# Performance work log

Measured on AMD Instinct MI355X. Metric: run time of the kernel, lower is better.

## Reference

```python
import jax, jax.numpy as jnp
import numpy as np
import math

B = 512
EMB = 512
CLASSNUM = 70722
M = 0.4
H = 0.333
S = 64.0
EPS = 1e-3


def setup_inputs() -> dict:
    key = jax.random.key(0)
    k1, k2, k3, k4, k5 = jax.random.split(key, 5)
    embbedings = jax.random.normal(k1, (B, EMB), dtype=jnp.float32)
    # feature norms: positive, realistic range ~[1, 30)
    norms = jax.random.uniform(k2, (B, 1), dtype=jnp.float32) * 29.0 + 1.0
    label = jax.random.randint(k3, (B,), 0, CLASSNUM, dtype=jnp.int64)
    class_sample_num_ = jax.random.uniform(k4, (B,), dtype=jnp.float32) * 9.0 + 1.0
    kernel = jax.random.normal(k5, (EMB, CLASSNUM), dtype=jnp.float32)
    return {
        "embbedings": embbedings,
        "norms": norms,
        "label": label,
        "class_sample_num_": class_sample_num_,
        "kernel": kernel,
    }


def reference(embbedings, norms, label, class_sample_num_, kernel):
    # l2-normalize kernel columns (axis=0)
    kernel_norm = kernel / jnp.linalg.norm(kernel, axis=0, keepdims=True)
    cosine = jnp.matmul(embbedings, kernel_norm)  # [B, C]
    cosine = jnp.clip(cosine, -1.0 + EPS, 1.0 - EPS)

    # detached margin scaler path (torch uses .detach / no_grad)
    safe_norms = jnp.clip(norms, 0.001, 100.0)
    safe_norms = safe_norms / (class_sample_num_[:, None] + 0.001)
    safe_norms = jnp.clip(safe_norms, 0.001, 100.0)
    safe_norms = jax.lax.stop_gradient(safe_norms)

    mean = jnp.mean(safe_norms)
    std = jnp.std(safe_norms, ddof=1)  # torch.std is unbiased
    # t_alpha = 1.0 => batch stats are exactly this batch's mean/std
    batch_mean, batch_std = mean, std

    margin_scaler = (safe_norms - batch_mean) / (batch_std + EPS)
    margin_scaler = jnp.clip(margin_scaler * H, -1.0, 1.0)  # [B, 1]
    ms = margin_scaler[:, 0]  # [B]

    rows = jnp.arange(B)
    lab = label.astype(jnp.int32)

    # angular margin: theta_m = clip(theta + onehot * (-m*ms))
    theta = jnp.arccos(cosine)
    theta = theta.at[rows, lab].add(-M * ms)
    theta_m = jnp.clip(theta, EPS, math.pi - EPS)
    cosine2 = jnp.cos(theta_m)

    # additive margin at the label column: g_add = m + m*ms
    cosine2 = cosine2.at[rows, lab].add(-(M + M * ms))

    return cosine2 * S
```

## Files before the change

kernel.cpp:

```cpp
#include <hip/hip_runtime.h>
#include <math.h>

#define CLASSNUM 70722
#define BATCH 512
#define EMBD 512
#define M_C 0.4f
#define H_C 0.333f
#define S_C 64.0f
#define EPS_C 0.001f
#define PI_F 3.14159265358979f

typedef __bf16 bf16_t;
typedef __bf16 bf16x4 __attribute__((ext_vector_type(4)));
typedef __bf16 bf16x8 __attribute__((ext_vector_type(8)));
typedef float f32x4 __attribute__((ext_vector_type(4)));

__device__ __forceinline__ float clampf(float x, float lo, float hi) {
    return fminf(fmaxf(x, lo), hi);
}

__global__ __launch_bounds__(256) void prep_lab_kernel(
    const float* __restrict__ emb, const float* __restrict__ norms,
    const float* __restrict__ csn, const int* __restrict__ label,
    const float* __restrict__ kmat, bf16_t* __restrict__ Aws,
    float* __restrict__ labout)
{
    __shared__ float red[256];
    const int tid = threadIdx.x;
    const int bi = blockIdx.x;

    if (bi < 128) {
        const int G = bi * 256 + tid;
        const int kt = G >> 11;
        const int rem = G & 2047;
        const int rg = rem >> 6;
        const int lane = rem & 63;
        const int row = rg * 16 + (lane & 15);
        const int k0 = kt * 32 + (lane >> 4) * 8;
        const float* src = emb + row * EMBD + k0;
        const float4 v0 = *(const float4*)src;
        const float4 v1 = *(const float4*)(src + 4);
        bf16x8 bw;
        bw[0] = (bf16_t)v0.x; bw[1] = (bf16_t)v0.y;
        bw[2] = (bf16_t)v0.z; bw[3] = (bf16_t)v0.w;
        bw[4] = (bf16_t)v1.x; bw[5] = (bf16_t)v1.y;
        bw[6] = (bf16_t)v1.z; bw[7] = (bf16_t)v1.w;
        *(bf16x8*)(Aws + (size_t)G * 8) = bw;
        return;
    }

    const int b = bi - 128;

    float s0, s1;
    {
        float sn = clampf(norms[tid], 0.001f, 100.0f);
        sn = sn / (csn[tid] + 0.001f);
        s0 = clampf(sn, 0.001f, 100.0f);
    }
    {
        float sn = clampf(norms[tid + 256], 0.001f, 100.0f);
        sn = sn / (csn[tid + 256] + 0.001f);
        s1 = clampf(sn, 0.001f, 100.0f);
    }
    red[tid] = s0 + s1;
    __syncthreads();
    for (int off = 128; off > 0; off >>= 1) {
        if (tid < off) red[tid] += red[tid + off];
        __syncthreads();
    }
    const float mean = red[0] * (1.0f / 512.0f);
    __syncthreads();
    const float d0 = s0 - mean, d1 = s1 - mean;
    red[tid] = d0 * d0 + d1 * d1;
    __syncthreads();
    for (int off = 128; off > 0; off >>= 1) {
        if (tid < off) red[tid] += red[tid + off];
        __syncthreads();
    }
    const float stdv = sqrtf(red[0] * (1.0f / 511.0f));
    __syncthreads();

    const int lab = label[b];
    const float* col = kmat + lab;
    const float* e = emb + b * EMBD;
    float dot = 0.0f, ss = 0.0f;
#pragma unroll
    for (int k = tid; k < EMBD; k += 256) {
        const float kv = col[(size_t)k * CLASSNUM];
        const float ev = e[k];
        dot = fmaf(ev, kv, dot);
        ss  = fmaf(kv, kv, ss);
    }
    red[tid] = dot;
    __syncthreads();
    for (int off = 128; off > 0; off >>= 1) {
        if (tid < off) red[tid] += red[tid + off];
        __syncthreads();
    }
    const float dotT = red[0];
    __syncthreads();
    red[tid] = ss;
    __syncthreads();
    for (int off = 128; off > 0; off >>= 1) {
        if (tid < off) red[tid] += red[tid + off];
        __syncthreads();
    }
    if (tid == 0) {
        const float ssT = red[0];
        float c = dotT / sqrtf(ssT);
        c = clampf(c, -1.0f + EPS_C, 1.0f - EPS_C);
        float snb = clampf(norms[b], 0.001f, 100.0f);
        snb = snb / (csn[b] + 0.001f);
        snb = clampf(snb, 0.001f, 100.0f);
        const float msv = clampf((snb - mean) / (stdv + EPS_C) * H_C, -1.0f, 1.0f);
        float th = acosf(c) - M_C * msv;
        th = clampf(th, EPS_C, PI_F - EPS_C);
        labout[b] = (cosf(th) - (M_C + M_C * msv)) * S_C;
    }
}


#define LOADB4(t, dst) do {                                             \
    const size_t ko_ = (size_t)((t) * 32) * CLASSNUM;                   \
    _Pragma("unroll")                                                   \
    for (int j_ = 0; j_ < 4; ++j_)                                      \
        dst[j_] = bp[ko_ + (size_t)j_ * CLASSNUM];                      \
} while (0)

#define LOADA4(t, af) do {                                              \
    const bf16x8* ap_ = (const bf16x8*)Aws                              \
        + (((t) * 32 + wave * 4) * 64 + lane);                          \
    _Pragma("unroll")                                                   \
    for (int mi_ = 0; mi_ < 4; ++mi_) af[mi_] = ap_[mi_ * 64];          \
} while (0)

#define CVTW(src, buf) do {                                             \
    bf16x4 w_;                                                          \
    _Pragma("unroll")                                                   \
    for (int j_ = 0; j_ < 4; ++j_) {                                    \
        const float v_ = src[j_];                                       \
        ssq = fmaf(v_, v_, ssq);                                        \
        w_[j_] = (bf16_t)v_;                                            \
    }                                                                   \
    *(bf16x4*)&Blds[buf][c * 40 + kg * 4] = w_;                         \
} while (0)

#define MFMA16(af, buf) do {                                            \
    bf16x8 bfr_[4];                                                     \
    _Pragma("unroll")                                                   \
    for (int ni_ = 0; ni_ < 4; ++ni_)                                   \
        bfr_[ni_] = *(const bf16x8*)                                    \
            &Blds[buf][(ni_ * 16 + r16) * 40 + quad * 8];               \
    _Pragma("unroll")                                                   \
    for (int mi_ = 0; mi_ < 4; ++mi_)                                   \
        _Pragma("unroll")                                               \
        for (int ni_ = 0; ni_ < 4; ++ni_)                               \
            acc[mi_][ni_] = __builtin_amdgcn_mfma_f32_16x16x32_bf16(    \
                af[mi_], bfr_[ni_], acc[mi_][ni_], 0, 0, 0);            \
} while (0)

#define BARRIER() do {                                                  \
    asm volatile("s_waitcnt lgkmcnt(0)" ::: "memory");                  \
    __builtin_amdgcn_s_barrier();                                       \
} while (0)

__global__ __launch_bounds__(512, 4) void gemm_kernel(
    const bf16_t* __restrict__ Aws, const float* __restrict__ Kmat,
    const int* __restrict__ label, const float* __restrict__ labout,
    float* __restrict__ out)
{
    __shared__ bf16_t Blds[2][64 * 40];
    __shared__ float red[512];
    __shared__ float invn_s[64];
    __shared__ int   lab_s[BATCH];
    __shared__ float lo_s[BATCH];

    const int tid  = threadIdx.x;
    const int lane = tid & 63;
    const int wave = tid >> 6;
    const int r16  = lane & 15;
    const int quad = lane >> 4;

    const int nwg = (CLASSNUM + 63) / 64;
    const int q_ = nwg >> 3, r_ = nwg & 7;
    const int xcd = blockIdx.x & 7, idx = blockIdx.x >> 3;
    const int nb = (xcd < r_) ? (xcd * (q_ + 1) + idx)
                              : (r_ * (q_ + 1) + (xcd - r_) * q_ + idx);
    const int n0 = nb * 64;

    lab_s[tid] = label[tid];
    lo_s[tid]  = labout[tid];

    const int c  = tid & 63;
    const int kg = tid >> 6;
    int cg = n0 + c;
    const bool cv = (cg < CLASSNUM);
    if (!cv) cg = CLASSNUM - 1;
    const float* bp = Kmat + (size_t)(kg * 4) * CLASSNUM + cg;

    f32x4 acc[4][4];
    const f32x4 zero = {0.0f, 0.0f, 0.0f, 0.0f};
#pragma unroll
    for (int i = 0; i < 4; ++i)
#pragma unroll
        for (int j = 0; j < 4; ++j) acc[i][j] = zero;
    float ssq = 0.0f;

    float bv0[4], bv1[4];

    LOADB4(0, bv0);
    LOADB4(1, bv1);
    CVTW(bv0, 0);
    BARRIER();

#pragma unroll 1
    for (int p = 0; p < 8; ++p) {
        {
            bf16x8 af[4];
            LOADA4(2 * p, af);
            if (p < 7) LOADB4(2 * p + 2, bv0);
            MFMA16(af, 0);
            CVTW(bv1, 1);
            BARRIER();
        }
        {
            bf16x8 af[4];
            LOADA4(2 * p + 1, af);
            if (p < 7) LOADB4(2 * p + 3, bv1);
            MFMA16(af, 1);
            if (p < 7) CVTW(bv0, 0);
            BARRIER();
        }
    }

    red[tid] = ssq;
    __syncthreads();
    if (tid < 64) {
        float s = 0.0f;
#pragma unroll
        for (int g = 0; g < 8; ++g) s += red[tid + g * 64];
        invn_s[tid] = (s > 0.0f) ? (1.0f / sqrtf(s)) : 0.0f;
    }
    __syncthreads();

#pragma unroll
    for (int mi = 0; mi < 4; ++mi) {
#pragma unroll
        for (int rr = 0; rr < 4; ++rr) {
            const int row = wave * 64 + mi * 16 + quad * 4 + rr;
            const int labc = lab_s[row];
            const float lov = lo_s[row];
            float* orow = out + (size_t)row * CLASSNUM;
#pragma unroll
            for (int ni = 0; ni < 4; ++ni) {
                const int col_loc = ni * 16 + r16;
                const int col = n0 + col_loc;
                if (col < CLASSNUM) {
                    const float cc = clampf(acc[mi][ni][rr] * invn_s[col_loc],
                                            -1.0f + EPS_C, 1.0f - EPS_C);
                    float v = cc * S_C;
                    if (labc == col) v = lov;
                    orow[col] = v;
                }
            }
        }
    }
}

extern "C" void kernel_launch(void* const* d_in, const int* in_sizes, int n_in,
                              void* d_out, int out_size, void* d_ws, size_t ws_size,
                              hipStream_t stream)
{
    const float* emb   = (const float*)d_in[0];
    const float* norms = (const float*)d_in[1];
    const int*   label = (const int*)d_in[2];
    const float* csn   = (const float*)d_in[3];
    const float* kmat  = (const float*)d_in[4];
    float* out = (float*)d_out;

    const size_t A_BYTES = (size_t)BATCH * EMBD * sizeof(bf16_t);
    if (ws_size < A_BYTES + 4096) return;
    bf16_t* Aws   = (bf16_t*)d_ws;
    float* labout = (float*)((char*)d_ws + A_BYTES);

    prep_lab_kernel<<<128 + BATCH, 256, 0, stream>>>(
        emb, norms, csn, label, kmat, Aws, labout);
    const int nblk = (CLASSNUM + 63) / 64;
    gemm_kernel<<<nblk, 512, 0, stream>>>(Aws, kmat, label, labout, out);
}
```

Measured before the change: 317.0 us.

## Move label-column margin into GEMM epilogue, prefetch A, setprio, nontemporal stores

Shrinks the prep kernel to a single stats block plus the bf16 conversion of A. It computes the per-row margin scaler once, instead of each of 512 blocks redoing the batch reduction and label-column dot. The label-column fp32 dot and margin are now computed inside the GEMM blocks that own that column, overlapping the prep work. Also adds A-fragment register prefetch one step ahead, s_setprio around the MFMA bursts, and nontemporal output stores. Extra per-block label scans and strided column reads in the epilogue add some latency to affected blocks.

```diff
diff --git a/kernel.cpp b/kernel.cpp
--- a/kernel.cpp
+++ b/kernel.cpp
@@ -19,18 +19,46 @@
     return fminf(fmaxf(x, lo), hi);
 }
 
-__global__ __launch_bounds__(256) void prep_lab_kernel(
+__global__ __launch_bounds__(256) void prep_kernel(
     const float* __restrict__ emb, const float* __restrict__ norms,
-    const float* __restrict__ csn, const int* __restrict__ label,
-    const float* __restrict__ kmat, bf16_t* __restrict__ Aws,
-    float* __restrict__ labout)
+    const float* __restrict__ csn, bf16_t* __restrict__ Aws,
+    float* __restrict__ msw)
 {
-    __shared__ float red[256];
+    __shared__ float sred[256];
     const int tid = threadIdx.x;
-    const int bi = blockIdx.x;
-
-    if (bi < 128) {
-        const int G = bi * 256 + tid;
+    if (blockIdx.x == 0) {
+        float s0, s1;
+        {
+            float sn = clampf(norms[tid], 0.001f, 100.0f);
+            sn = sn / (csn[tid] + 0.001f);
+            s0 = clampf(sn, 0.001f, 100.0f);
+        }
+        {
+            float sn = clampf(norms[tid + 256], 0.001f, 100.0f);
+            sn = sn / (csn[tid + 256] + 0.001f);
+            s1 = clampf(sn, 0.001f, 100.0f);
+        }
+        sred[tid] = s0 + s1;
+        __syncthreads();
+        for (int off = 128; off > 0; off >>= 1) {
+            if (tid < off) sred[tid] += sred[tid + off];
+            __syncthreads();
+        }
+        const float mean = sred[0] * (1.0f / 512.0f);
+        __syncthreads();
+        const float d0 = s0 - mean, d1 = s1 - mean;
+        sred[tid] = d0 * d0 + d1 * d1;
+        __syncthreads();
+        for (int off = 128; off > 0; off >>= 1) {
+            if (tid < off) sred[tid] += sred[tid + off];
+            __syncthreads();
+        }
+        const float stdv = sqrtf(sred[0] * (1.0f / 511.0f));
+        const float inv = 1.0f / (stdv + EPS_C);
+        msw[tid]       = clampf(d0 * inv * H_C, -1.0f, 1.0f);
+        msw[tid + 256] = clampf(d1 * inv * H_C, -1.0f, 1.0f);
+    } else {
+        const int G = (blockIdx.x - 1) * 256 + tid;
         const int kt = G >> 11;
         const int rem = G & 2047;
         const int rg = rem >> 6;
@@ -46,76 +74,6 @@
         bw[4] = (bf16_t)v1.x; bw[5] = (bf16_t)v1.y;
         bw[6] = (bf16_t)v1.z; bw[7] = (bf16_t)v1.w;
         *(bf16x8*)(Aws + (size_t)G * 8) = bw;
-        return;
-    }
-
-    const int b = bi - 128;
-
-    float s0, s1;
-    {
-        float sn = clampf(norms[tid], 0.001f, 100.0f);
-        sn = sn / (csn[tid] + 0.001f);
-        s0 = clampf(sn, 0.001f, 100.0f);
-    }
-    {
-        float sn = clampf(norms[tid + 256], 0.001f, 100.0f);
-        sn = sn / (csn[tid + 256] + 0.001f);
-        s1 = clampf(sn, 0.001f, 100.0f);
-    }
-    red[tid] = s0 + s1;
-    __syncthreads();
-    for (int off = 128; off > 0; off >>= 1) {
-        if (tid < off) red[tid] += red[tid + off];
-        __syncthreads();
-    }
-    const float mean = red[0] * (1.0f / 512.0f);
-    __syncthreads();
-    const float d0 = s0 - mean, d1 = s1 - mean;
-    red[tid] = d0 * d0 + d1 * d1;
-    __syncthreads();
-    for (int off = 128; off > 0; off >>= 1) {
-        if (tid < off) red[tid] += red[tid + off];
-        __syncthreads();
-    }
-    const float stdv = sqrtf(red[0] * (1.0f / 511.0f));
-    __syncthreads();
-
-    const int lab = label[b];
-    const float* col = kmat + lab;
-    const float* e = emb + b * EMBD;
-    float dot = 0.0f, ss = 0.0f;
-#pragma unroll
-    for (int k = tid; k < EMBD; k += 256) {
-        const float kv = col[(size_t)k * CLASSNUM];
-        const float ev = e[k];
-        dot = fmaf(ev, kv, dot);
-        ss  = fmaf(kv, kv, ss);
-    }
-    red[tid] = dot;
-    __syncthreads();
-    for (int off = 128; off > 0; off >>= 1) {
-        if (tid < off) red[tid] += red[tid + off];
-        __syncthreads();
-    }
-    const float dotT = red[0];
-    __syncthreads();
-    red[tid] = ss;
-    __syncthreads();
-    for (int off = 128; off > 0; off >>= 1) {
-        if (tid < off) red[tid] += red[tid + off];
-        __syncthreads();
-    }
-    if (tid == 0) {
-        const float ssT = red[0];
-        float c = dotT / sqrtf(ssT);
-        c = clampf(c, -1.0f + EPS_C, 1.0f - EPS_C);
-        float snb = clampf(norms[b], 0.001f, 100.0f);
-        snb = snb / (csn[b] + 0.001f);
-        snb = clampf(snb, 0.001f, 100.0f);
-        const float msv = clampf((snb - mean) / (stdv + EPS_C) * H_C, -1.0f, 1.0f);
-        float th = acosf(c) - M_C * msv;
-        th = clampf(th, EPS_C, PI_F - EPS_C);
-        labout[b] = (cosf(th) - (M_C + M_C * msv)) * S_C;
     }
 }
 
@@ -151,12 +109,14 @@
     for (int ni_ = 0; ni_ < 4; ++ni_)                                   \
         bfr_[ni_] = *(const bf16x8*)                                    \
             &Blds[buf][(ni_ * 16 + r16) * 40 + quad * 8];               \
+    __builtin_amdgcn_s_setprio(1);                                      \
     _Pragma("unroll")                                                   \
     for (int mi_ = 0; mi_ < 4; ++mi_)                                   \
         _Pragma("unroll")                                               \
         for (int ni_ = 0; ni_ < 4; ++ni_)                               \
             acc[mi_][ni_] = __builtin_amdgcn_mfma_f32_16x16x32_bf16(    \
                 af[mi_], bfr_[ni_], acc[mi_][ni_], 0, 0, 0);            \
+    __builtin_amdgcn_s_setprio(0);                                      \
 } while (0)
 
 #define BARRIER() do {                                                  \
@@ -166,8 +126,8 @@
 
 __global__ __launch_bounds__(512, 4) void gemm_kernel(
     const bf16_t* __restrict__ Aws, const float* __restrict__ Kmat,
-    const int* __restrict__ label, const float* __restrict__ labout,
-    float* __restrict__ out)
+    const float* __restrict__ emb, const int* __restrict__ label,
+    const float* __restrict__ msw, float* __restrict__ out)
 {
     __shared__ bf16_t Blds[2][64 * 40];
     __shared__ float red[512];
@@ -189,13 +149,11 @@
     const int n0 = nb * 64;
 
     lab_s[tid] = label[tid];
-    lo_s[tid]  = labout[tid];
 
     const int c  = tid & 63;
     const int kg = tid >> 6;
     int cg = n0 + c;
-    const bool cv = (cg < CLASSNUM);
-    if (!cv) cg = CLASSNUM - 1;
+    if (cg >= CLASSNUM) cg = CLASSNUM - 1;
     const float* bp = Kmat + (size_t)(kg * 4) * CLASSNUM + cg;
 
     f32x4 acc[4][4];
@@ -207,28 +165,30 @@
     float ssq = 0.0f;
 
     float bv0[4], bv1[4];
+    bf16x8 af[4];
 
     LOADB4(0, bv0);
     LOADB4(1, bv1);
+    LOADA4(0, af);
     CVTW(bv0, 0);
     BARRIER();
 
 #pragma unroll 1
     for (int p = 0; p < 8; ++p) {
         {
-            bf16x8 af[4];
-            LOADA4(2 * p, af);
             if (p < 7) LOADB4(2 * p + 2, bv0);
             MFMA16(af, 0);
+            LOADA4(2 * p + 1, af);
             CVTW(bv1, 1);
             BARRIER();
         }
         {
-            bf16x8 af[4];
-            LOADA4(2 * p + 1, af);
             if (p < 7) LOADB4(2 * p + 3, bv1);
             MFMA16(af, 1);
-            if (p < 7) CVTW(bv0, 0);
+            if (p < 7) {
+                LOADA4(2 * p + 2, af);
+                CVTW(bv0, 0);
+            }
             BARRIER();
         }
     }
@@ -240,6 +200,34 @@
 #pragma unroll
         for (int g = 0; g < 8; ++g) s += red[tid + g * 64];
         invn_s[tid] = (s > 0.0f) ? (1.0f / sqrtf(s)) : 0.0f;
+    }
+
+#pragma unroll 1
+    for (int b = wave; b < BATCH; b += 8) {
+        const int lc = lab_s[b];
+        if (lc >= n0 && lc < n0 + 64) {
+            const float* col = Kmat + lc;
+            const float* e = emb + b * EMBD;
+            float dot = 0.0f, ss = 0.0f;
+#pragma unroll
+            for (int k = lane; k < EMBD; k += 64) {
+                const float kv = col[(size_t)k * CLASSNUM];
+                dot = fmaf(e[k], kv, dot);
+                ss  = fmaf(kv, kv, ss);
+            }
+            for (int off = 32; off > 0; off >>= 1) {
+                dot += __shfl_down(dot, off);
+                ss  += __shfl_down(ss, off);
+            }
+            if (lane == 0) {
+                float cc = dot / sqrtf(ss);
+                cc = clampf(cc, -1.0f + EPS_C, 1.0f - EPS_C);
+                const float msv = msw[b];
+                float th = acosf(cc) - M_C * msv;
+                th = clampf(th, EPS_C, PI_F - EPS_C);
+                lo_s[b] = (cosf(th) - (M_C + M_C * msv)) * S_C;
+            }
+        }
     }
     __syncthreads();
 
@@ -260,7 +248,7 @@
                                             -1.0f + EPS_C, 1.0f - EPS_C);
                     float v = cc * S_C;
                     if (labc == col) v = lov;
-                    orow[col] = v;
+                    __builtin_nontemporal_store(v, &orow[col]);
                 }
             }
         }
@@ -280,11 +268,10 @@
 
     const size_t A_BYTES = (size_t)BATCH * EMBD * sizeof(bf16_t);
     if (ws_size < A_BYTES + 4096) return;
-    bf16_t* Aws   = (bf16_t*)d_ws;
-    float* labout = (float*)((char*)d_ws + A_BYTES);
-
-    prep_lab_kernel<<<128 + BATCH, 256, 0, stream>>>(
-        emb, norms, csn, label, kmat, Aws, labout);
+    bf16_t* Aws = (bf16_t*)d_ws;
+    float* msw  = (float*)((char*)d_ws + A_BYTES);
+
+    prep_kernel<<<129, 256, 0, stream>>>(emb, norms, csn, Aws, msw);
     const int nblk = (CLASSNUM + 63) / 64;
-    gemm_kernel<<<nblk, 512, 0, stream>>>(Aws, kmat, label, labout, out);
-}
+    gemm_kernel<<<nblk, 512, 0, stream>>>(Aws, kmat, emb, label, msw, out);
+}
```

New measurement: 367.3 us. +15.9%, slower.
